# Performance work log

Hardware: AMD Instinct MI355X
Metric: run time of the kernel (lower is better)

Reference implementation:

```python
import jax, jax.numpy as jnp
import numpy as np

B, N, DIM, H, DH = 2, 2048, 1024, 16, 64

def setup_inputs() -> dict:
    key = jax.random.key(0)
    ks = jax.random.split(key, 7)
    s = 0.02
    return {
        "x": jax.random.normal(ks[0], (B, N, DIM), jnp.float32),
        "pos_emb": jax.random.normal(ks[1], (N, DH), jnp.float32),
        "Wq": jax.random.normal(ks[2], (DIM, H * DH), jnp.float32) * s,
        "Wk": jax.random.normal(ks[3], (DIM, H * DH), jnp.float32) * s,
        "Wv": jax.random.normal(ks[4], (DIM, H * DH), jnp.float32) * s,
        "Wo": jax.random.normal(ks[5], (H * DH, DIM), jnp.float32) * s,
        "bo": jnp.zeros((DIM,), jnp.float32),
    }

def _rotate_half(t):
    t1, t2 = jnp.split(t, 2, axis=-1)
    return jnp.concatenate([-t2, t1], axis=-1)

def _apply_rotary(t, angles):
    # t: [b,h,n,d], angles: [n,d]
    cos = jnp.cos(angles)[None, None]
    sin = jnp.sin(angles)[None, None]
    return t * cos + _rotate_half(t) * sin

def reference(x, pos_emb, Wq, Wk, Wv, Wo, bo):
    b, n, _ = x.shape
    scale = DH ** -0.5
    def split_heads(t):  # [b,n,h*d] -> [b,h,n,d]
        return t.reshape(b, n, H, DH).transpose(0, 2, 1, 3)
    q = split_heads(x @ Wq) * scale
    k = split_heads(x @ Wk)
    v = split_heads(x @ Wv)
    q = _apply_rotary(q, pos_emb)
    k = _apply_rotary(k, pos_emb)
    sim = jnp.einsum('bhid,bhjd->bhij', q, k)
    mask_value = -jnp.finfo(sim.dtype).max
    causal_mask = jnp.triu(jnp.ones((n, n), dtype=bool), 1)
    sim = jnp.where(causal_mask, mask_value, sim)
    attn = jax.nn.softmax(sim, axis=-1)
    out = jnp.einsum('bhij,bhjd->bhid', attn, v)
    out = out.transpose(0, 2, 1, 3).reshape(b, n, H * DH)
    return out @ Wo + bo
```

## Files before the change

kernel.cpp:

```cpp
#include <hip/hip_runtime.h>

#define B_   2
#define N_   2048
#define DIM_ 1024
#define H_   16
#define DH_  64
#define M_   (B_*N_)
#define QKVN (3*DIM_)

typedef __attribute__((ext_vector_type(8)))  short short8;
typedef __attribute__((ext_vector_type(4)))  float floatx4;
typedef __attribute__((ext_vector_type(16))) float floatx16;

__device__ inline unsigned short f2b(float f) {
  union { float f; unsigned u; } v; v.f = f;
  unsigned r = v.u + 0x7fffu + ((v.u >> 16) & 1u);
  return (unsigned short)(r >> 16);
}

__device__ inline unsigned cvtpk(float a, float b) {
  unsigned d;
  asm("v_cvt_pk_bf16_f32 %0, %1, %2" : "=v"(d) : "v"(a), "v"(b));
  return d;
}

__device__ inline floatx4 mfma16(short8 a, short8 b, floatx4 c) {
  return __builtin_amdgcn_mfma_f32_16x16x32_bf16(a, b, c, 0, 0, 0);
}
__device__ inline floatx16 mfma32(short8 a, short8 b, floatx16 c) {
  return __builtin_amdgcn_mfma_f32_32x32x16_bf16(a, b, c, 0, 0, 0);
}

__device__ inline int swz(int row, int byteoff) {
  return row * 64 + (((byteoff) ^ ((row & 7) << 4)) >> 1);
}

__device__ inline void gl_lds16(const void* g, void* l) {
  __builtin_amdgcn_global_load_lds((const __attribute__((address_space(1))) void*)g,
                                   (__attribute__((address_space(3))) void*)l, 16, 0, 0);
}

__device__ inline short8 u4_to_s8(unsigned a, unsigned b, unsigned c, unsigned d) {
  union { unsigned u[4]; short8 s; } v;
  v.u[0] = a; v.u[1] = b; v.u[2] = c; v.u[3] = d;
  return v.s;
}

__global__ void cast_x_kernel(const float* __restrict__ x, unsigned short* __restrict__ xb) {
  int i = blockIdx.x * 256 + threadIdx.x;
  float4 v = ((const float4*)x)[i];
  ushort4 o;
  o.x = f2b(v.x); o.y = f2b(v.y); o.z = f2b(v.z); o.w = f2b(v.w);
  ((ushort4*)xb)[i] = o;
}

__global__ void trig_kernel(const float* __restrict__ pos, float* __restrict__ cs) {
  int i = blockIdx.x * 256 + threadIdx.x;
  float a = pos[i];
  float2 v; v.x = cosf(a); v.y = sinf(a);
  ((float2*)cs)[i] = v;
}

__global__ void transpose_w_kernel(const float* __restrict__ W0, const float* __restrict__ W1,
                                   const float* __restrict__ W2, const float* __restrict__ W3,
                                   unsigned short* __restrict__ T0, unsigned short* __restrict__ T1,
                                   unsigned short* __restrict__ T2, unsigned short* __restrict__ T3) {
  int z = blockIdx.z;
  const float* W = (z == 0) ? W0 : (z == 1) ? W1 : (z == 2) ? W2 : W3;
  unsigned short* T = (z == 0) ? T0 : (z == 1) ? T1 : (z == 2) ? T2 : T3;
  __shared__ float tile[32][33];
  int x = threadIdx.x, y = threadIdx.y;
  int bx = blockIdx.x * 32, by = blockIdx.y * 32;
  #pragma unroll
  for (int i = 0; i < 32; i += 8)
    tile[y + i][x] = W[(size_t)(by + y + i) * 1024 + bx + x];
  __syncthreads();
  #pragma unroll
  for (int i = 0; i < 32; i += 8)
    T[(size_t)(bx + y + i) * 1024 + by + x] = f2b(tile[x][y + i]);
}

template <int MODE>
__global__ __launch_bounds__(256) void gemm_bt_kernel(
    const unsigned short* __restrict__ A, const unsigned short* __restrict__ BT,
    float* __restrict__ C, const float* __restrict__ bias,
    const float* __restrict__ cs,
    unsigned short* __restrict__ qb, unsigned short* __restrict__ kb,
    unsigned short* __restrict__ vtb,
    int M, int N, int K)
{
  __shared__ __align__(16) unsigned short SH[2][4096];
  unsigned short* As = &SH[0][0];
  unsigned short* Bs = &SH[1][0];
  int t = threadIdx.x;
  int lane = t & 63, wave = t >> 6;
  int wr = (wave >> 1) * 64, wc = (wave & 1) * 64;

  const unsigned short* Ab = A  + (size_t)(blockIdx.y * 128) * K;
  const unsigned short* Bb = BT + (size_t)(blockIdx.x * 128) * K;

  int sA = wave * 2;
  int grow = (lane >> 2), gcol = (lane & 3) * 8;
  const unsigned short* gA0 = Ab + (size_t)((sA    ) * 16 + grow) * K + gcol;
  const unsigned short* gA1 = Ab + (size_t)((sA + 1) * 16 + grow) * K + gcol;
  const unsigned short* gB0 = Bb + (size_t)((sA    ) * 16 + grow) * K + gcol;
  const unsigned short* gB1 = Bb + (size_t)((sA + 1) * 16 + grow) * K + gcol;
  unsigned short* lA0 = &As[(sA    ) * 512];
  unsigned short* lA1 = &As[(sA + 1) * 512];
  unsigned short* lB0 = &Bs[(sA    ) * 512];
  unsigned short* lB1 = &Bs[(sA + 1) * 512];

  floatx4 acc[4][4];
  #pragma unroll
  for (int i = 0; i < 4; ++i)
    #pragma unroll
    for (int j = 0; j < 4; ++j)
      acc[i][j] = (floatx4){0.f, 0.f, 0.f, 0.f};

  int nk = K >> 5;
  for (int kt = 0; kt < nk; ++kt) {
    if (kt) __syncthreads();
    int ko = kt * 32;
    gl_lds16(gA0 + ko, lA0);
    gl_lds16(gA1 + ko, lA1);
    gl_lds16(gB0 + ko, lB0);
    gl_lds16(gB1 + ko, lB1);
    __syncthreads();
    short8 af[4], bf[4];
    #pragma unroll
    for (int fi = 0; fi < 4; ++fi)
      af[fi] = *(const short8*)&As[(wr + fi * 16 + (lane & 15)) * 32 + (lane >> 4) * 8];
    #pragma unroll
    for (int fj = 0; fj < 4; ++fj)
      bf[fj] = *(const short8*)&Bs[(wc + fj * 16 + (lane & 15)) * 32 + (lane >> 4) * 8];
    __builtin_amdgcn_s_setprio(1);
    #pragma unroll
    for (int fi = 0; fi < 4; ++fi)
      #pragma unroll
      for (int fj = 0; fj < 4; ++fj)
        acc[fi][fj] = mfma16(af[fi], bf[fj], acc[fi][fj]);
    __builtin_amdgcn_s_setprio(0);
  }

  int lane15 = lane & 15;
  int row0 = blockIdx.y * 128 + wr + (lane >> 4) * 4;

  if constexpr (MODE == 0) {
    int col0 = blockIdx.x * 128 + wc + lane15;
    #pragma unroll
    for (int fi = 0; fi < 4; ++fi) {
      #pragma unroll
      for (int fj = 0; fj < 4; ++fj) {
        int col = col0 + fj * 16;
        float bv = bias ? bias[col] : 0.f;
        #pragma unroll
        for (int r = 0; r < 4; ++r) {
          int row = row0 + fi * 16 + r;
          C[(size_t)row * N + col] = acc[fi][fj][r] + bv;
        }
      }
    }
  } else {
    __syncthreads();
    unsigned short* ep = &SH[0][0];
    int colbase = blockIdx.x * 128 + wc;
    int region = colbase >> 10;
    int bb = (blockIdx.y * 128) >> 11;
    if (region < 2) {
      const float qs = (region == 0) ? 0.18033688011112042f : 1.0f;
      unsigned short* dstb = (region == 0) ? qb : kb;
      int h = (colbase >> 6) & 15;
      #pragma unroll
      for (int h2 = 0; h2 < 2; ++h2) {
        #pragma unroll
        for (int fi2 = 0; fi2 < 2; ++fi2) {
          int fi = h2 * 2 + fi2;
          #pragma unroll
          for (int fj = 0; fj < 4; ++fj) {
            int d = fj * 16 + lane15;
            float sgn = (fj < 2) ? -1.f : 1.f;
            #pragma unroll
            for (int r = 0; r < 4; ++r) {
              int n = (row0 + fi * 16 + r) & 2047;
              float2 csv = *(const float2*)&cs[((size_t)n * 64 + d) * 2];
              float a = acc[fi][fj][r], p = acc[fi][fj ^ 2][r];
              int nloc = fi2 * 16 + ((lane >> 4) & 3) * 4 + r;
              ep[wave * 2048 + nloc * 64 + d] = f2b((a * csv.x + sgn * p * csv.y) * qs);
            }
          }
        }
        __syncthreads();
        {
          int r2 = lane >> 1, half = lane & 1;
          int n_glob = blockIdx.y * 128 + wr + h2 * 32 + r2;
          int nn = n_glob & 2047;
          unsigned short* dst = dstb + (((size_t)(bb * 16 + h)) * 2048 + nn) * 64 + half * 32;
          const unsigned short* srcp = ep + wave * 2048 + r2 * 64 + half * 32;
          #pragma unroll
          for (int c = 0; c < 4; ++c)
            *(int4*)(dst + c * 8) = *(const int4*)(srcp + c * 8);
        }
        __syncthreads();
      }
    } else {
      int n0 = (blockIdx.y * 128) & 2047;
      int hA = ((blockIdx.x * 128) >> 6) & 15;
      #pragma unroll
      for (int nh = 0; nh < 2; ++nh) {
        if ((wave >> 1) == nh) {
          #pragma unroll
          for (int fi = 0; fi < 4; ++fi) {
            #pragma unroll
            for (int fj = 0; fj < 4; ++fj) {
              int d = fj * 16 + lane15;
              int sw = (d & 7) << 3;
              #pragma unroll
              for (int r = 0; r < 4; ++r) {
                int nl = fi * 16 + ((lane >> 4) & 3) * 4 + r;
                ep[(wave & 1) * 4096 + d * 64 + (nl ^ sw)] = f2b(acc[fi][fj][r]);
              }
            }
          }
        }
        __syncthreads();
        {
          int hh = t >> 7, d = (t >> 1) & 63, half = t & 1;
          int sw = (d & 7) << 3;
          const unsigned short* srcp = ep + hh * 4096 + d * 64;
          unsigned short* dst = vtb + (((size_t)(bb * 16 + hA + hh)) * 64 + d) * 2048
                                    + n0 + nh * 64 + half * 32;
          #pragma unroll
          for (int c = 0; c < 4; ++c) {
            int off = (half * 32 + c * 8) ^ sw;
            *(int4*)(dst + c * 8) = *(const int4*)(srcp + off);
          }
        }
        __syncthreads();
      }
    }
  }
}

__global__ __launch_bounds__(256) void attn_kernel(
    const unsigned short* __restrict__ qg, const unsigned short* __restrict__ kg,
    const unsigned short* __restrict__ vtg, unsigned short* __restrict__ ctx)
{
  __shared__ __align__(16) unsigned short KV[4][4096];

  int bid = blockIdx.x;
  int bh  = bid & 31;
  int qc  = (bid < 256) ? (15 - (bid >> 5)) : ((bid - 256) >> 5);
  int t = threadIdx.x, lane = t & 63, wave = t >> 6;
  int lane31 = lane & 31, hi = lane >> 5;
  bool hib = (hi != 0);
  int b = bh >> 4, h = bh & 15;

  const unsigned short* kp = kg  + (size_t)bh * N_ * DH_;
  const unsigned short* vp = vtg + (size_t)bh * 64 * (size_t)N_;

  int srow = t >> 2;
  int scol = (t & 3) * 16;
  int4 kreg0, kreg1, vreg0, vreg1;

#define LOAD_TILE(KV0) do {                                                    \
    kreg0 = *(const int4*)(kp + (size_t)((KV0) + srow) * 64 + scol);           \
    kreg1 = *(const int4*)(kp + (size_t)((KV0) + srow) * 64 + scol + 8);       \
    vreg0 = *(const int4*)(vp + (size_t)srow * N_ + (KV0) + scol);             \
    vreg1 = *(const int4*)(vp + (size_t)srow * N_ + (KV0) + scol + 8);         \
  } while (0)
#define STORE_TILE(BUF) do {                                                   \
    *(int4*)&KV[(BUF)][swz(srow, (t & 3) * 32)]          = kreg0;              \
    *(int4*)&KV[(BUF)][swz(srow, (t & 3) * 32 + 16)]     = kreg1;              \
    *(int4*)&KV[2 + (BUF)][swz(srow, (t & 3) * 32)]      = vreg0;              \
    *(int4*)&KV[2 + (BUF)][swz(srow, (t & 3) * 32 + 16)] = vreg1;              \
  } while (0)

  int q0 = qc * 128;
  int nt = (qc + 1) * 2;
  int qw0 = q0 + wave * 32;
  int qr  = qw0 + lane31;

  short8 qf[4];
  {
    const unsigned short* qrp = qg + ((size_t)bh * N_ + qr) * DH_;
    #pragma unroll
    for (int ks = 0; ks < 4; ++ks)
      qf[ks] = *(const short8*)(qrp + ks * 16 + hi * 8);
  }

  LOAD_TILE(0);
  STORE_TILE(0);

  floatx16 oa0 = (floatx16)(0.f), oa1 = (floatx16)(0.f);
  float lr = 0.f;

  for (int kt = 0; kt < nt; ++kt) {
    __syncthreads();
    int kv0 = kt * 64;
    bool more = (kt + 1 < nt);
    if (more) LOAD_TILE(kv0 + 64);

    bool active = (kv0 <= qw0 + 31);
    if (active) {
      const unsigned short* Kb = KV[kt & 1];
      const unsigned short* Vb = KV[2 + (kt & 1)];

      floatx16 sa0 = (floatx16)(0.f), sa1 = (floatx16)(0.f);
      __builtin_amdgcn_s_setprio(1);
      #pragma unroll
      for (int ks = 0; ks < 4; ++ks) {
        int bo = ks * 32 + hi * 16;
        short8 kf0 = *(const short8*)&Kb[swz(lane31, bo)];
        short8 kf1 = *(const short8*)&Kb[swz(32 + lane31, bo)];
        sa0 = mfma32(kf0, qf[ks], sa0);
        sa1 = mfma32(kf1, qf[ks], sa1);
      }
      __builtin_amdgcn_s_setprio(0);

      if (kv0 + 63 > qw0) {
        #pragma unroll
        for (int r = 0; r < 16; ++r) {
          int kvA = kv0 + ((r & 3) + 8 * (r >> 2) + 4 * hi);
          if (kvA > qr)      sa0[r] = -3.0e38f;
          if (kvA + 32 > qr) sa1[r] = -3.0e38f;
        }
      }

      float ps = 0.f;
      #pragma unroll
      for (int r = 0; r < 16; ++r) {
        float p0 = exp2f(sa0[r]); sa0[r] = p0; ps += p0;
        float p1 = exp2f(sa1[r]); sa1[r] = p1; ps += p1;
      }
      ps += __shfl_xor(ps, 32);
      lr += ps;

      #pragma unroll
      for (int kvb = 0; kvb < 2; ++kvb) {
        floatx16 sv = (kvb == 0) ? sa0 : sa1;
        unsigned pk0 = cvtpk(sv[0],  sv[1]),  pk1 = cvtpk(sv[2],  sv[3]);
        unsigned pk2 = cvtpk(sv[4],  sv[5]),  pk3 = cvtpk(sv[6],  sv[7]);
        unsigned pk4 = cvtpk(sv[8],  sv[9]),  pk5 = cvtpk(sv[10], sv[11]);
        unsigned pk6 = cvtpk(sv[12], sv[13]), pk7 = cvtpk(sv[14], sv[15]);
        unsigned t0 = hib ? pk0 : pk2, t1 = hib ? pk1 : pk3;
        unsigned t2 = hib ? pk4 : pk6, t3 = hib ? pk5 : pk7;
        unsigned r0 = (unsigned)__shfl_xor((int)t0, 32);
        unsigned r1 = (unsigned)__shfl_xor((int)t1, 32);
        unsigned r2 = (unsigned)__shfl_xor((int)t2, 32);
        unsigned r3 = (unsigned)__shfl_xor((int)t3, 32);
        unsigned o0 = hib ? pk2 : pk0, o1 = hib ? pk3 : pk1;
        unsigned o2 = hib ? pk6 : pk4, o3 = hib ? pk7 : pk5;
        short8 pa = u4_to_s8(hib ? r0 : o0, hib ? r1 : o1, hib ? o0 : r0, hib ? o1 : r1);
        short8 pb = u4_to_s8(hib ? r2 : o2, hib ? r3 : o3, hib ? o2 : r2, hib ? o3 : r3);
        int ksA = kvb * 2, ksB = kvb * 2 + 1;
        short8 v00 = *(const short8*)&Vb[swz(lane31,      ksA * 32 + hi * 16)];
        short8 v01 = *(const short8*)&Vb[swz(32 + lane31, ksA * 32 + hi * 16)];
        short8 v10 = *(const short8*)&Vb[swz(lane31,      ksB * 32 + hi * 16)];
        short8 v11 = *(const short8*)&Vb[swz(32 + lane31, ksB * 32 + hi * 16)];
        __builtin_amdgcn_s_setprio(1);
        oa0 = mfma32(v00, pa, oa0);
        oa1 = mfma32(v01, pa, oa1);
        oa0 = mfma32(v10, pb, oa0);
        oa1 = mfma32(v11, pb, oa1);
        __builtin_amdgcn_s_setprio(0);
      }
    }

    if (more) STORE_TILE((kt + 1) & 1);
  }

  __syncthreads();
  {
    float inv = 1.0f / lr;
    int qrow = wave * 32 + lane31;
    #pragma unroll
    for (int db = 0; db < 2; ++db) {
      floatx16 ov = (db == 0) ? oa0 : oa1;
      #pragma unroll
      for (int a = 0; a < 4; ++a) {
        unsigned w0 = cvtpk(ov[4 * a + 0] * inv, ov[4 * a + 1] * inv);
        unsigned w1 = cvtpk(ov[4 * a + 2] * inv, ov[4 * a + 3] * inv);
        int byteoff = 64 * db + 16 * a + 8 * hi;
        uint2 val; val.x = w0; val.y = w1;
        *(uint2*)&KV[qrow >> 6][(qrow & 63) * 64 + ((byteoff ^ ((qrow & 7) << 4)) >> 1)] = val;
      }
    }
  }
  __syncthreads();
  {
    int r = t >> 1, halfo = (t & 1) * 64;
    const unsigned short* srow_ = &KV[r >> 6][(r & 63) * 64];
    unsigned short* dst = ctx + (size_t)(b * N_ + q0 + r) * DIM_ + h * 64 + (halfo >> 1);
    #pragma unroll
    for (int c = 0; c < 4; ++c) {
      int byteo = halfo + c * 16;
      int4 v = *(const int4*)&srow_[(byteo ^ ((r & 7) << 4)) >> 1];
      *(int4*)(dst + c * 8) = v;
    }
  }
#undef LOAD_TILE
#undef STORE_TILE
}

extern "C" void kernel_launch(void* const* d_in, const int* in_sizes, int n_in,
                              void* d_out, int out_size, void* d_ws, size_t ws_size,
                              hipStream_t stream)
{
  const float* x   = (const float*)d_in[0];
  const float* pos = (const float*)d_in[1];
  const float* Wq  = (const float*)d_in[2];
  const float* Wk  = (const float*)d_in[3];
  const float* Wv  = (const float*)d_in[4];
  const float* Wo  = (const float*)d_in[5];
  const float* bo  = (const float*)d_in[6];
  float* out = (float*)d_out;

  char* w = (char*)d_ws;
  size_t off = 0;
  auto alloc = [&](size_t bytes) {
    char* p = w + off;
    off += (bytes + 255) & ~(size_t)255;
    return p;
  };
  unsigned short* xb  = (unsigned short*)alloc((size_t)M_ * DIM_ * 2);
  unsigned short* WT  = (unsigned short*)alloc((size_t)QKVN * DIM_ * 2);
  unsigned short* WoT = (unsigned short*)alloc((size_t)DIM_ * DIM_ * 2);
  float* cs = (float*)alloc((size_t)N_ * DH_ * 2 * 4);
  unsigned short* qb  = (unsigned short*)alloc((size_t)B_ * H_ * N_ * DH_ * 2);
  unsigned short* kb  = (unsigned short*)alloc((size_t)B_ * H_ * N_ * DH_ * 2);
  unsigned short* vtb = (unsigned short*)alloc((size_t)B_ * H_ * N_ * DH_ * 2);
  unsigned short* ctx = (unsigned short*)alloc((size_t)M_ * DIM_ * 2);

  cast_x_kernel<<<(M_ * DIM_ / 4) / 256, 256, 0, stream>>>(x, xb);
  trig_kernel<<<(N_ * DH_) / 256, 256, 0, stream>>>(pos, cs);
  transpose_w_kernel<<<dim3(32, 32, 4), dim3(32, 8), 0, stream>>>(
      Wq, Wk, Wv, Wo,
      WT, WT + (size_t)DIM_ * DIM_, WT + (size_t)2 * DIM_ * DIM_, WoT);
  gemm_bt_kernel<1><<<dim3(QKVN / 128, M_ / 128), 256, 0, stream>>>(
      xb, WT, nullptr, nullptr, cs, qb, kb, vtb, M_, QKVN, DIM_);
  attn_kernel<<<512, 256, 0, stream>>>(qb, kb, vtb, ctx);
  gemm_bt_kernel<0><<<dim3(DIM_ / 128, M_ / 128), 256, 0, stream>>>(
      ctx, WoT, out, bo, nullptr, nullptr, nullptr, nullptr, M_, DIM_, DIM_);
}
```

Baseline: 227.9 us.

## Split attention KV tile across wave pairs and reduce partial outputs in LDS

Doubles the attention block to 512 threads, so each pair of waves shares a 32-row query slice and each wave handles one 32-key half of every 64-key tile. The partial P·V accumulators and row sums from the second wave are written to shared memory, then combined and normalized by the first wave. This aims to raise wave-level parallelism and latency hiding per CU. The cost is extra LDS traffic, added barriers for the final reduction, and idle waves in the epilogue.

```diff
diff --git a/kernel.cpp b/kernel.cpp
--- a/kernel.cpp
+++ b/kernel.cpp
@@ -241,16 +241,18 @@
   }
 }
 
-__global__ __launch_bounds__(256) void attn_kernel(
+__global__ __launch_bounds__(512, 4) void attn_kernel(
     const unsigned short* __restrict__ qg, const unsigned short* __restrict__ kg,
     const unsigned short* __restrict__ vtg, unsigned short* __restrict__ ctx)
 {
   __shared__ __align__(16) unsigned short KV[4][4096];
+  __shared__ float lrbuf[4][32];
 
   int bid = blockIdx.x;
   int bh  = bid & 31;
   int qc  = (bid < 256) ? (15 - (bid >> 5)) : ((bid - 256) >> 5);
   int t = threadIdx.x, lane = t & 63, wave = t >> 6;
+  int s = wave >> 1, kvh = wave & 1;
   int lane31 = lane & 31, hi = lane >> 5;
   bool hib = (hi != 0);
   int b = bh >> 4, h = bh & 15;
@@ -258,26 +260,22 @@
   const unsigned short* kp = kg  + (size_t)bh * N_ * DH_;
   const unsigned short* vp = vtg + (size_t)bh * 64 * (size_t)N_;
 
-  int srow = t >> 2;
-  int scol = (t & 3) * 16;
-  int4 kreg0, kreg1, vreg0, vreg1;
+  int srow = t >> 3;
+  int sc16 = (t & 7) * 16;
+  int4 kreg, vreg;
 
 #define LOAD_TILE(KV0) do {                                                    \
-    kreg0 = *(const int4*)(kp + (size_t)((KV0) + srow) * 64 + scol);           \
-    kreg1 = *(const int4*)(kp + (size_t)((KV0) + srow) * 64 + scol + 8);       \
-    vreg0 = *(const int4*)(vp + (size_t)srow * N_ + (KV0) + scol);             \
-    vreg1 = *(const int4*)(vp + (size_t)srow * N_ + (KV0) + scol + 8);         \
+    kreg = *(const int4*)(kp + (size_t)((KV0) + srow) * 64 + (sc16 >> 1));     \
+    vreg = *(const int4*)(vp + (size_t)srow * N_ + (KV0) + (sc16 >> 1));       \
   } while (0)
 #define STORE_TILE(BUF) do {                                                   \
-    *(int4*)&KV[(BUF)][swz(srow, (t & 3) * 32)]          = kreg0;              \
-    *(int4*)&KV[(BUF)][swz(srow, (t & 3) * 32 + 16)]     = kreg1;              \
-    *(int4*)&KV[2 + (BUF)][swz(srow, (t & 3) * 32)]      = vreg0;              \
-    *(int4*)&KV[2 + (BUF)][swz(srow, (t & 3) * 32 + 16)] = vreg1;              \
+    *(int4*)&KV[(BUF)][swz(srow, sc16)]     = kreg;                            \
+    *(int4*)&KV[2 + (BUF)][swz(srow, sc16)] = vreg;                            \
   } while (0)
 
   int q0 = qc * 128;
   int nt = (qc + 1) * 2;
-  int qw0 = q0 + wave * 32;
+  int qw0 = q0 + s * 32;
   int qr  = qw0 + lane31;
 
   short8 qf[4];
@@ -300,86 +298,100 @@
     bool more = (kt + 1 < nt);
     if (more) LOAD_TILE(kv0 + 64);
 
-    bool active = (kv0 <= qw0 + 31);
+    int kvbase = kv0 + kvh * 32;
+    bool active = (kvbase <= qw0 + 31);
     if (active) {
       const unsigned short* Kb = KV[kt & 1];
       const unsigned short* Vb = KV[2 + (kt & 1)];
 
-      floatx16 sa0 = (floatx16)(0.f), sa1 = (floatx16)(0.f);
+      floatx16 sa = (floatx16)(0.f);
       __builtin_amdgcn_s_setprio(1);
       #pragma unroll
       for (int ks = 0; ks < 4; ++ks) {
-        int bo = ks * 32 + hi * 16;
-        short8 kf0 = *(const short8*)&Kb[swz(lane31, bo)];
-        short8 kf1 = *(const short8*)&Kb[swz(32 + lane31, bo)];
-        sa0 = mfma32(kf0, qf[ks], sa0);
-        sa1 = mfma32(kf1, qf[ks], sa1);
+        short8 kf = *(const short8*)&Kb[swz(kvh * 32 + lane31, ks * 32 + hi * 16)];
+        sa = mfma32(kf, qf[ks], sa);
       }
       __builtin_amdgcn_s_setprio(0);
 
-      if (kv0 + 63 > qw0) {
+      if (kvbase + 31 > qw0) {
         #pragma unroll
         for (int r = 0; r < 16; ++r) {
-          int kvA = kv0 + ((r & 3) + 8 * (r >> 2) + 4 * hi);
-          if (kvA > qr)      sa0[r] = -3.0e38f;
-          if (kvA + 32 > qr) sa1[r] = -3.0e38f;
+          int kvA = kvbase + ((r & 3) + 8 * (r >> 2) + 4 * hi);
+          if (kvA > qr) sa[r] = -3.0e38f;
         }
       }
 
       float ps = 0.f;
       #pragma unroll
       for (int r = 0; r < 16; ++r) {
-        float p0 = exp2f(sa0[r]); sa0[r] = p0; ps += p0;
-        float p1 = exp2f(sa1[r]); sa1[r] = p1; ps += p1;
+        float p = exp2f(sa[r]); sa[r] = p; ps += p;
       }
       ps += __shfl_xor(ps, 32);
       lr += ps;
 
-      #pragma unroll
-      for (int kvb = 0; kvb < 2; ++kvb) {
-        floatx16 sv = (kvb == 0) ? sa0 : sa1;
-        unsigned pk0 = cvtpk(sv[0],  sv[1]),  pk1 = cvtpk(sv[2],  sv[3]);
-        unsigned pk2 = cvtpk(sv[4],  sv[5]),  pk3 = cvtpk(sv[6],  sv[7]);
-        unsigned pk4 = cvtpk(sv[8],  sv[9]),  pk5 = cvtpk(sv[10], sv[11]);
-        unsigned pk6 = cvtpk(sv[12], sv[13]), pk7 = cvtpk(sv[14], sv[15]);
-        unsigned t0 = hib ? pk0 : pk2, t1 = hib ? pk1 : pk3;
-        unsigned t2 = hib ? pk4 : pk6, t3 = hib ? pk5 : pk7;
-        unsigned r0 = (unsigned)__shfl_xor((int)t0, 32);
-        unsigned r1 = (unsigned)__shfl_xor((int)t1, 32);
-        unsigned r2 = (unsigned)__shfl_xor((int)t2, 32);
-        unsigned r3 = (unsigned)__shfl_xor((int)t3, 32);
-        unsigned o0 = hib ? pk2 : pk0, o1 = hib ? pk3 : pk1;
-        unsigned o2 = hib ? pk6 : pk4, o3 = hib ? pk7 : pk5;
-        short8 pa = u4_to_s8(hib ? r0 : o0, hib ? r1 : o1, hib ? o0 : r0, hib ? o1 : r1);
-        short8 pb = u4_to_s8(hib ? r2 : o2, hib ? r3 : o3, hib ? o2 : r2, hib ? o3 : r3);
-        int ksA = kvb * 2, ksB = kvb * 2 + 1;
-        short8 v00 = *(const short8*)&Vb[swz(lane31,      ksA * 32 + hi * 16)];
-        short8 v01 = *(const short8*)&Vb[swz(32 + lane31, ksA * 32 + hi * 16)];
-        short8 v10 = *(const short8*)&Vb[swz(lane31,      ksB * 32 + hi * 16)];
-        short8 v11 = *(const short8*)&Vb[swz(32 + lane31, ksB * 32 + hi * 16)];
-        __builtin_amdgcn_s_setprio(1);
-        oa0 = mfma32(v00, pa, oa0);
-        oa1 = mfma32(v01, pa, oa1);
-        oa0 = mfma32(v10, pb, oa0);
-        oa1 = mfma32(v11, pb, oa1);
-        __builtin_amdgcn_s_setprio(0);
-      }
+      unsigned pk0 = cvtpk(sa[0],  sa[1]),  pk1 = cvtpk(sa[2],  sa[3]);
+      unsigned pk2 = cvtpk(sa[4],  sa[5]),  pk3 = cvtpk(sa[6],  sa[7]);
+      unsigned pk4 = cvtpk(sa[8],  sa[9]),  pk5 = cvtpk(sa[10], sa[11]);
+      unsigned pk6 = cvtpk(sa[12], sa[13]), pk7 = cvtpk(sa[14], sa[15]);
+      unsigned t0 = hib ? pk0 : pk2, t1 = hib ? pk1 : pk3;
+      unsigned t2 = hib ? pk4 : pk6, t3 = hib ? pk5 : pk7;
+      unsigned r0 = (unsigned)__shfl_xor((int)t0, 32);
+      unsigned r1 = (unsigned)__shfl_xor((int)t1, 32);
+      unsigned r2 = (unsigned)__shfl_xor((int)t2, 32);
+      unsigned r3 = (unsigned)__shfl_xor((int)t3, 32);
+      unsigned o0 = hib ? pk2 : pk0, o1 = hib ? pk3 : pk1;
+      unsigned o2 = hib ? pk6 : pk4, o3 = hib ? pk7 : pk5;
+      short8 pa = u4_to_s8(hib ? r0 : o0, hib ? r1 : o1, hib ? o0 : r0, hib ? o1 : r1);
+      short8 pb = u4_to_s8(hib ? r2 : o2, hib ? r3 : o3, hib ? o2 : r2, hib ? o3 : r3);
+
+      int vb0 = kvh * 64;
+      short8 v00 = *(const short8*)&Vb[swz(lane31,      vb0 + hi * 16)];
+      short8 v01 = *(const short8*)&Vb[swz(32 + lane31, vb0 + hi * 16)];
+      short8 v10 = *(const short8*)&Vb[swz(lane31,      vb0 + 32 + hi * 16)];
+      short8 v11 = *(const short8*)&Vb[swz(32 + lane31, vb0 + 32 + hi * 16)];
+      __builtin_amdgcn_s_setprio(1);
+      oa0 = mfma32(v00, pa, oa0);
+      oa1 = mfma32(v01, pa, oa1);
+      oa0 = mfma32(v10, pb, oa0);
+      oa1 = mfma32(v11, pb, oa1);
+      __builtin_amdgcn_s_setprio(0);
     }
 
     if (more) STORE_TILE((kt + 1) & 1);
   }
 
   __syncthreads();
-  {
-    float inv = 1.0f / lr;
-    int qrow = wave * 32 + lane31;
+  float* F = (float*)&KV[0][0];
+  int fsw = (lane31 & 7) << 2;
+  if (kvh == 1) {
+    #pragma unroll
+    for (int r = 0; r < 16; ++r) {
+      int d = (r & 3) + 8 * (r >> 2) + 4 * hi;
+      F[s * 2048 + lane31 * 64 + (d ^ fsw)]        = oa0[r];
+      F[s * 2048 + lane31 * 64 + ((32 + d) ^ fsw)] = oa1[r];
+    }
+    if (!hib) lrbuf[s][lane31] = lr;
+  }
+  __syncthreads();
+  if (kvh == 0) {
+    float inv = 1.0f / (lr + lrbuf[s][lane31]);
+    #pragma unroll
+    for (int r = 0; r < 16; ++r) {
+      int d = (r & 3) + 8 * (r >> 2) + 4 * hi;
+      oa0[r] = (oa0[r] + F[s * 2048 + lane31 * 64 + (d ^ fsw)])        * inv;
+      oa1[r] = (oa1[r] + F[s * 2048 + lane31 * 64 + ((32 + d) ^ fsw)]) * inv;
+    }
+  }
+  __syncthreads();
+  if (kvh == 0) {
+    int qrow = s * 32 + lane31;
     #pragma unroll
     for (int db = 0; db < 2; ++db) {
       floatx16 ov = (db == 0) ? oa0 : oa1;
       #pragma unroll
       for (int a = 0; a < 4; ++a) {
-        unsigned w0 = cvtpk(ov[4 * a + 0] * inv, ov[4 * a + 1] * inv);
-        unsigned w1 = cvtpk(ov[4 * a + 2] * inv, ov[4 * a + 3] * inv);
+        unsigned w0 = cvtpk(ov[4 * a + 0], ov[4 * a + 1]);
+        unsigned w1 = cvtpk(ov[4 * a + 2], ov[4 * a + 3]);
         int byteoff = 64 * db + 16 * a + 8 * hi;
         uint2 val; val.x = w0; val.y = w1;
         *(uint2*)&KV[qrow >> 6][(qrow & 63) * 64 + ((byteoff ^ ((qrow & 7) << 4)) >> 1)] = val;
@@ -388,12 +400,12 @@
   }
   __syncthreads();
   {
-    int r = t >> 1, halfo = (t & 1) * 64;
+    int r = t >> 2, q4 = (t & 3) * 32;
     const unsigned short* srow_ = &KV[r >> 6][(r & 63) * 64];
-    unsigned short* dst = ctx + (size_t)(b * N_ + q0 + r) * DIM_ + h * 64 + (halfo >> 1);
-    #pragma unroll
-    for (int c = 0; c < 4; ++c) {
-      int byteo = halfo + c * 16;
+    unsigned short* dst = ctx + (size_t)(b * N_ + q0 + r) * DIM_ + h * 64 + (q4 >> 1);
+    #pragma unroll
+    for (int c = 0; c < 2; ++c) {
+      int byteo = q4 + c * 16;
       int4 v = *(const int4*)&srow_[(byteo ^ ((r & 7) << 4)) >> 1];
       *(int4*)(dst + c * 8) = v;
     }
@@ -438,7 +450,7 @@
       WT, WT + (size_t)DIM_ * DIM_, WT + (size_t)2 * DIM_ * DIM_, WoT);
   gemm_bt_kernel<1><<<dim3(QKVN / 128, M_ / 128), 256, 0, stream>>>(
       xb, WT, nullptr, nullptr, cs, qb, kb, vtb, M_, QKVN, DIM_);
-  attn_kernel<<<512, 256, 0, stream>>>(qb, kb, vtb, ctx);
+  attn_kernel<<<512, 512, 0, stream>>>(qb, kb, vtb, ctx);
   gemm_bt_kernel<0><<<dim3(DIM_ / 128, M_ / 128), 256, 0, stream>>>(
       ctx, WoT, out, bo, nullptr, nullptr, nullptr, nullptr, M_, DIM_, DIM_);
 }
```

Result: faster. 214.2 us (-6.0%).
